# Kernel tuning notes

Measured on AMD Instinct MI355X. Metric: run time of the kernel, lower is better.

Reference implementation:

```python
import jax, jax.numpy as jnp
import numpy as np

B, S, D, H, FF = 2, 2048, 1024, 16, 4096
DH = D // H  # per-head dim = 64
EPS = 1e-5


def layer_norm(x, g, b):
    mu = jnp.mean(x, axis=-1, keepdims=True)
    var = jnp.mean((x - mu) ** 2, axis=-1, keepdims=True)
    return (x - mu) * jax.lax.rsqrt(var + EPS) * g + b


def setup_inputs() -> dict:
    key = jax.random.key(0)
    ks = jax.random.split(key, 12)
    s_in = 1.0 / np.sqrt(D)
    s_ff = 1.0 / np.sqrt(FF)
    return {
        "x": jax.random.normal(ks[0], (B, S, D), jnp.float32),
        # per-head projections stacked over heads: [H, D, DH]
        "Wq": jax.random.normal(ks[1], (H, D, DH), jnp.float32) * s_in,
        "bq": jnp.zeros((H, DH), jnp.float32),
        "Wk": jax.random.normal(ks[2], (H, D, DH), jnp.float32) * s_in,
        "bk": jnp.zeros((H, DH), jnp.float32),
        "Wv": jax.random.normal(ks[3], (H, D, DH), jnp.float32) * s_in,
        "bv": jnp.zeros((H, DH), jnp.float32),
        "ln1_g": jnp.ones((D,), jnp.float32),
        "ln1_b": jnp.zeros((D,), jnp.float32),
        "ln2_g": jnp.ones((D,), jnp.float32),
        "ln2_b": jnp.zeros((D,), jnp.float32),
        "W1": jax.random.normal(ks[4], (D, FF), jnp.float32) * s_in,
        "b1": jnp.zeros((FF,), jnp.float32),
        "W2": jax.random.normal(ks[5], (FF, D), jnp.float32) * s_ff,
        "b2": jnp.zeros((D,), jnp.float32),
    }


def reference(x, Wq, bq, Wk, bk, Wv, bv, ln1_g, ln1_b, ln2_g, ln2_b, W1, b1, W2, b2):
    # --- attention sub-block (pre-LN) ---
    h = layer_norm(x, ln1_g, ln1_b)                      # [B,S,D]
    q = jnp.einsum('bsd,hde->bhse', h, Wq) + bq[None, :, None, :]
    k = jnp.einsum('bsd,hde->bhse', h, Wk) + bk[None, :, None, :]
    v = jnp.einsum('bsd,hde->bhse', h, Wv) + bv[None, :, None, :]
    score = jnp.einsum('bhse,bhte->bhst', q, k) / jnp.sqrt(jnp.float32(DH))
    causal = jnp.tril(jnp.ones((S, S), bool))            # lower-triangular mask
    score = jnp.where(causal, score, -jnp.inf)
    attn = jax.nn.softmax(score, axis=-1)                # [B,H,S,S]
    o = jnp.einsum('bhst,bhte->bhse', attn, v)           # [B,H,S,DH]
    o = jnp.transpose(o, (0, 2, 1, 3)).reshape(B, S, D)  # concat heads
    x = x + o
    # --- FFN sub-block (pre-LN) ---
    h2 = layer_norm(x, ln2_g, ln2_b)
    f = jax.nn.gelu(h2 @ W1 + b1, approximate=False) @ W2 + b2
    return x + f
```

## Files before the change

kernel.cpp:

```cpp
#include <hip/hip_runtime.h>
#include <hip/hip_bf16.h>
#include <cstdint>
#include <cstddef>


typedef short bf16x8 __attribute__((ext_vector_type(8)));
typedef float f32x4 __attribute__((ext_vector_type(4)));

#define DEV static __device__ __forceinline__

DEV unsigned short f2bf(float f) {
  union { float fv; unsigned u; } a; a.fv = f;
  unsigned r = a.u + 0x7FFFu + ((a.u >> 16) & 1u);
  return (unsigned short)(r >> 16);
}

DEV void gload_lds16(const void* g, void* l) {
  __builtin_amdgcn_global_load_lds(
      (const __attribute__((address_space(1))) unsigned int*)g,
      (__attribute__((address_space(3))) unsigned int*)l,
      16, 0, 0);
}

__global__ __launch_bounds__(256) void k_transpose(const float* __restrict__ in,
                                                   unsigned short* __restrict__ out,
                                                   int R, int C,
                                                   long inBatchStride, long outBatchStride) {
  __shared__ float tile[32][33];
  long batch = blockIdx.z;
  int c0 = blockIdx.x * 32;
  int r0 = blockIdx.y * 32;
  const float* src = in + batch * inBatchStride;
  unsigned short* dst = out + batch * outBatchStride;
  int tx = threadIdx.x, ty = threadIdx.y;
  #pragma unroll
  for (int i = ty; i < 32; i += 8)
    tile[i][tx] = src[(long)(r0 + i) * C + (c0 + tx)];
  __syncthreads();
  #pragma unroll
  for (int i = ty; i < 32; i += 8)
    dst[(long)(c0 + i) * R + (r0 + tx)] = f2bf(tile[tx][i]);
}

__global__ void k_concat_bias(const float* __restrict__ bq, const float* __restrict__ bk,
                              const float* __restrict__ bv, float* __restrict__ out) {
  int i = blockIdx.x * 256 + threadIdx.x;
  if (i < 1024) out[i] = bq[i];
  else if (i < 2048) out[i] = bk[i - 1024];
  else if (i < 3072) out[i] = bv[i - 2048];
}

__global__ __launch_bounds__(256) void k_ln_bf16(const float* __restrict__ x,
                                                 const float* __restrict__ g,
                                                 const float* __restrict__ b,
                                                 unsigned short* __restrict__ out) {
  int row = blockIdx.x;
  const float* xr = x + (size_t)row * 1024;
  int t = threadIdx.x;
  float4 v = *(const float4*)(xr + t * 4);
  float s = v.x + v.y + v.z + v.w;
  float s2 = v.x * v.x + v.y * v.y + v.z * v.z + v.w * v.w;
  for (int off = 32; off > 0; off >>= 1) {
    s  += __shfl_down(s,  off, 64);
    s2 += __shfl_down(s2, off, 64);
  }
  __shared__ float ws1[4], ws2[4];
  __shared__ float mu_s, rs_s;
  int wid = t >> 6, lane = t & 63;
  if (lane == 0) { ws1[wid] = s; ws2[wid] = s2; }
  __syncthreads();
  if (t == 0) {
    float S1 = ws1[0] + ws1[1] + ws1[2] + ws1[3];
    float S2 = ws2[0] + ws2[1] + ws2[2] + ws2[3];
    float mu = S1 * (1.0f / 1024.0f);
    float var = S2 * (1.0f / 1024.0f) - mu * mu;
    mu_s = mu;
    rs_s = rsqrtf(var + 1e-5f);
  }
  __syncthreads();
  float mu = mu_s, rs = rs_s;
  float4 gv = *(const float4*)(g + t * 4);
  float4 bv = *(const float4*)(b + t * 4);
  ushort4 o;
  o.x = f2bf((v.x - mu) * rs * gv.x + bv.x);
  o.y = f2bf((v.y - mu) * rs * gv.y + bv.y);
  o.z = f2bf((v.z - mu) * rs * gv.z + bv.z);
  o.w = f2bf((v.w - mu) * rs * gv.w + bv.w);
  *(ushort4*)(out + (size_t)row * 1024 + t * 4) = o;
}

template <int EPI>
__global__ __launch_bounds__(256) void k_gemm_bt(const unsigned short* __restrict__ A,
                                                 const unsigned short* __restrict__ Bt,
                                                 const float* __restrict__ bias,
                                                 void* __restrict__ Cout,
                                                 int M, int N, int K,
                                                 int nbx, int nby, int kparts) {
  __shared__ __align__(16) unsigned short As[128 * 64];
  __shared__ __align__(16) unsigned short Bs[128 * 64];
  int tid = threadIdx.x;

  int nwg = nbx * nby * kparts;
  int flat = blockIdx.x;
  int swz = (flat & 7) * (nwg >> 3) + (flat >> 3);
  int bx = swz % nbx;
  int rest = swz / nbx;
  int by = rest % nby;
  int kp = rest / nby;
  int col0 = bx * 128;
  int row0 = by * 128;
  int kLen = K / kparts;
  int kBeg = kp * kLen;

  int wid = tid >> 6, lane = tid & 63;
  int wr = wid >> 1, wc = wid & 1;
  int lrow = lane & 15;
  int g = lane >> 4;
  int s_row = tid >> 3;
  int s_scol = ((tid & 7) ^ (s_row & 7)) * 8;

  f32x4 acc[4][4];
  f32x4 zero = {0.f, 0.f, 0.f, 0.f};
  #pragma unroll
  for (int m = 0; m < 4; ++m)
    #pragma unroll
    for (int n = 0; n < 4; ++n) acc[m][n] = zero;

  for (int k0 = kBeg; k0 < kBeg + kLen; k0 += 64) {
    #pragma unroll
    for (int i = 0; i < 4; ++i) {
      int r = i * 32 + s_row;
      gload_lds16(A  + (size_t)(row0 + r) * K + k0 + s_scol, (char*)As + i * 4096 + tid * 16);
      gload_lds16(Bt + (size_t)(col0 + r) * K + k0 + s_scol, (char*)Bs + i * 4096 + tid * 16);
    }
    __syncthreads();
    bf16x8 af[4][2], bf[4][2];
    #pragma unroll
    for (int m = 0; m < 4; ++m) {
      int ra = wr * 64 + m * 16 + lrow;
      #pragma unroll
      for (int kk = 0; kk < 2; ++kk) {
        int byteoff = ra * 128 + (((kk * 4 + g) ^ (lrow & 7)) << 4);
        af[m][kk] = *(const bf16x8*)((const char*)As + byteoff);
      }
    }
    #pragma unroll
    for (int n = 0; n < 4; ++n) {
      int rb = wc * 64 + n * 16 + lrow;
      #pragma unroll
      for (int kk = 0; kk < 2; ++kk) {
        int byteoff = rb * 128 + (((kk * 4 + g) ^ (lrow & 7)) << 4);
        bf[n][kk] = *(const bf16x8*)((const char*)Bs + byteoff);
      }
    }
    #pragma unroll
    for (int m = 0; m < 4; ++m)
      #pragma unroll
      for (int n = 0; n < 4; ++n)
        #pragma unroll
        for (int kk = 0; kk < 2; ++kk)
          acc[m][n] = __builtin_amdgcn_mfma_f32_16x16x32_bf16(af[m][kk], bf[n][kk], acc[m][n], 0, 0, 0);
    __syncthreads();
  }

  int rbase = row0 + wr * 64 + g * 4;
  int cbase = col0 + wc * 64 + lrow;
  #pragma unroll
  for (int m = 0; m < 4; ++m) {
    #pragma unroll
    for (int n = 0; n < 4; ++n) {
      int col = cbase + n * 16;
      float bia = bias[col];
      #pragma unroll
      for (int j = 0; j < 4; ++j) {
        int row = rbase + m * 16 + j;
        float v = acc[m][n][j];
        if constexpr (EPI == 0) {
          ((unsigned short*)Cout)[(size_t)row * N + col] = f2bf(v + bia);
        } else if constexpr (EPI == 1) {
          float u = v + bia;
          float gel = 0.5f * u * (1.0f + erff(u * 0.70710678118f));
          ((unsigned short*)Cout)[(size_t)row * N + col] = f2bf(gel);
        } else {
          float u = v + (kp == 0 ? bia : 0.0f);
          atomicAdd((float*)Cout + (size_t)row * N + col, u);
        }
      }
    }
  }
}

__global__ __launch_bounds__(256) void k_flash_attn(const unsigned short* __restrict__ qkv,
                                                    const float* __restrict__ x,
                                                    float* __restrict__ out) {
  int blk = blockIdx.x;
  int pairIdx = blk & 15;
  int bh = blk >> 4;
  int b = bh >> 4, h = bh & 15;
  const int LDQ = 3072;
  int tb = b * 2048;
  int qcol = h * 64, kcol = 1024 + h * 64, vcol = 2048 + h * 64;
  int tid = threadIdx.x, wid = tid >> 6, lane = tid & 63;
  int lrow = lane & 15;
  int g = lane >> 4;
  int kgrp = g * 8;

  __shared__ __align__(16) unsigned short Ks[2][64 * 64];
  __shared__ __align__(16) unsigned short Vt[2][64 * 64];
  __shared__ __align__(16) unsigned short Pl[4][16 * 64];

  int s_row = tid >> 3;
  int s_srccol = ((tid & 7) ^ ((tid >> 3) & 7)) * 8;

  unsigned short* myP = &Pl[wid][0];
  f32x4 zero = {0.f, 0.f, 0.f, 0.f};

  for (int half = 0; half < 2; ++half) {
    int qt = (half == 0) ? pairIdx : 31 - pairIdx;
    int q0 = qt * 64;
    int nkv = qt + 1;

    bf16x8 aq[2];
    #pragma unroll
    for (int kk = 0; kk < 2; ++kk)
      aq[kk] = *(const bf16x8*)(qkv + (size_t)(tb + q0 + wid * 16 + lrow) * LDQ + qcol + kk * 32 + kgrp);

    f32x4 oacc[4];
    #pragma unroll
    for (int e = 0; e < 4; ++e) oacc[e] = zero;
    float mrun[4], lrun[4];
    #pragma unroll
    for (int r = 0; r < 4; ++r) { mrun[r] = -1e30f; lrun[r] = 0.0f; }

    int cur = 0;
    bf16x8 vreg[2];

    #pragma unroll
    for (int i = 0; i < 2; ++i)
      gload_lds16(qkv + (size_t)(tb + i * 32 + s_row) * LDQ + kcol + s_srccol,
                  (char*)Ks[0] + i * 4096 + tid * 16);
    #pragma unroll
    for (int i = 0; i < 2; ++i) {
      int chunk = i * 256 + tid;
      vreg[i] = *(const bf16x8*)(qkv + (size_t)(tb + (chunk >> 3)) * LDQ + vcol + (chunk & 7) * 8);
    }
    #pragma unroll
    for (int i = 0; i < 2; ++i) {
      int chunk = i * 256 + tid;
      int t = chunk >> 3, e0 = (chunk & 7) * 8;
      #pragma unroll
      for (int jj = 0; jj < 8; ++jj) {
        int e = e0 + jj;
        int byteoff = e * 128 + ((((t >> 3) ^ (e & 7) ^ (e >> 3)) & 7) << 4) + (t & 7) * 2;
        *(unsigned short*)((char*)Vt[0] + byteoff) = (unsigned short)vreg[i][jj];
      }
    }

    for (int j = 0; j < nkv; ++j) {
      __syncthreads();
      int nxt = cur ^ 1;
      bool pf = (j + 1 < nkv);
      if (pf) {
        #pragma unroll
        for (int i = 0; i < 2; ++i)
          gload_lds16(qkv + (size_t)(tb + (j + 1) * 64 + i * 32 + s_row) * LDQ + kcol + s_srccol,
                      (char*)Ks[nxt] + i * 4096 + tid * 16);
        #pragma unroll
        for (int i = 0; i < 2; ++i) {
          int chunk = i * 256 + tid;
          vreg[i] = *(const bf16x8*)(qkv + (size_t)(tb + (j + 1) * 64 + (chunk >> 3)) * LDQ + vcol + (chunk & 7) * 8);
        }
      }

      f32x4 sacc[4];
      #pragma unroll
      for (int n = 0; n < 4; ++n) sacc[n] = zero;
      __builtin_amdgcn_s_setprio(1);
      #pragma unroll
      for (int n = 0; n < 4; ++n) {
        int trow = n * 16 + lrow;
        #pragma unroll
        for (int kk = 0; kk < 2; ++kk) {
          int byteoff = trow * 128 + (((kk * 4 + g) ^ (trow & 7)) << 4);
          bf16x8 bk = *(const bf16x8*)((const char*)Ks[cur] + byteoff);
          sacc[n] = __builtin_amdgcn_mfma_f32_16x16x32_bf16(aq[kk], bk, sacc[n], 0, 0, 0);
        }
      }
      __builtin_amdgcn_s_setprio(0);

      bool diag = (j == qt);
      float pv[4][4];
      #pragma unroll
      for (int r = 0; r < 4; ++r) {
        int sg = q0 + wid * 16 + g * 4 + r;
        float mx = -1e30f;
        #pragma unroll
        for (int n = 0; n < 4; ++n) {
          float sv = sacc[n][r] * 0.125f;
          int tg = j * 64 + n * 16 + lrow;
          if (diag && tg > sg) sv = -1e30f;
          pv[r][n] = sv;
          mx = fmaxf(mx, sv);
        }
        #pragma unroll
        for (int off = 1; off < 16; off <<= 1) mx = fmaxf(mx, __shfl_xor(mx, off, 64));
        float mnew = fmaxf(mrun[r], mx);
        float esc = __expf(mrun[r] - mnew);
        float rsum = 0.f;
        #pragma unroll
        for (int n = 0; n < 4; ++n) {
          float p = __expf(pv[r][n] - mnew);
          pv[r][n] = p;
          rsum += p;
        }
        #pragma unroll
        for (int off = 1; off < 16; off <<= 1) rsum += __shfl_xor(rsum, off, 64);
        lrun[r] = lrun[r] * esc + rsum;
        mrun[r] = mnew;
        #pragma unroll
        for (int e = 0; e < 4; ++e) oacc[e][r] *= esc;
      }

      if (pf) {
        #pragma unroll
        for (int i = 0; i < 2; ++i) {
          int chunk = i * 256 + tid;
          int t = chunk >> 3, e0 = (chunk & 7) * 8;
          #pragma unroll
          for (int jj = 0; jj < 8; ++jj) {
            int e = e0 + jj;
            int byteoff = e * 128 + ((((t >> 3) ^ (e & 7) ^ (e >> 3)) & 7) << 4) + (t & 7) * 2;
            *(unsigned short*)((char*)Vt[nxt] + byteoff) = (unsigned short)vreg[i][jj];
          }
        }
      }

      #pragma unroll
      for (int r = 0; r < 4; ++r) {
        int q = g * 4 + r;
        #pragma unroll
        for (int n = 0; n < 4; ++n) {
          int t = n * 16 + lrow;
          int byteoff = q * 128 + ((((t >> 3) ^ (q & 7)) & 7) << 4) + (t & 7) * 2;
          *(unsigned short*)((char*)myP + byteoff) = f2bf(pv[r][n]);
        }
      }

      __builtin_amdgcn_s_setprio(1);
      #pragma unroll
      for (int kk = 0; kk < 2; ++kk) {
        int pbyte = lrow * 128 + (((kk * 4 + g) ^ (lrow & 7)) << 4);
        bf16x8 ap = *(const bf16x8*)((const char*)myP + pbyte);
        #pragma unroll
        for (int e = 0; e < 4; ++e) {
          int erow = e * 16 + lrow;
          int vbyte = erow * 128 + ((((kk * 4 + g) ^ (erow & 7) ^ (erow >> 3)) & 7) << 4);
          bf16x8 bv = *(const bf16x8*)((const char*)Vt[cur] + vbyte);
          oacc[e] = __builtin_amdgcn_mfma_f32_16x16x32_bf16(ap, bv, oacc[e], 0, 0, 0);
        }
      }
      __builtin_amdgcn_s_setprio(0);
      cur = nxt;
    }

    #pragma unroll
    for (int r = 0; r < 4; ++r) {
      float inv = 1.0f / lrun[r];
      int row = tb + q0 + wid * 16 + g * 4 + r;
      #pragma unroll
      for (int e = 0; e < 4; ++e) {
        size_t idx = (size_t)row * 1024 + h * 64 + e * 16 + lrow;
        out[idx] = x[idx] + oacc[e][r] * inv;
      }
    }
  }
}

extern "C" void kernel_launch(void* const* d_in, const int* in_sizes, int n_in,
                              void* d_out, int out_size, void* d_ws, size_t ws_size,
                              hipStream_t stream) {
  (void)in_sizes; (void)n_in; (void)out_size; (void)ws_size;
  const float* x    = (const float*)d_in[0];
  const float* Wq   = (const float*)d_in[1];
  const float* bq   = (const float*)d_in[2];
  const float* Wk   = (const float*)d_in[3];
  const float* bk   = (const float*)d_in[4];
  const float* Wv   = (const float*)d_in[5];
  const float* bv   = (const float*)d_in[6];
  const float* ln1g = (const float*)d_in[7];
  const float* ln1b = (const float*)d_in[8];
  const float* ln2g = (const float*)d_in[9];
  const float* ln2b = (const float*)d_in[10];
  const float* W1   = (const float*)d_in[11];
  const float* b1   = (const float*)d_in[12];
  const float* W2   = (const float*)d_in[13];
  const float* b2   = (const float*)d_in[14];
  float* out = (float*)d_out;
  char* ws = (char*)d_ws;

  unsigned short* h1    = (unsigned short*)(ws + 0);
  unsigned short* wqkvT = (unsigned short*)(ws + 8388608);
  unsigned short* w1T   = (unsigned short*)(ws + 14680064);
  unsigned short* w2T   = (unsigned short*)(ws + 23068672);
  float*          bqkv  = (float*)(ws + 31457280);
  unsigned short* qkv   = (unsigned short*)(ws + 33554432);
  unsigned short* fbuf  = (unsigned short*)(ws + 33554432);

  dim3 tb(32, 8);
  k_transpose<<<dim3(2, 32, 16), tb, 0, stream>>>(Wq, wqkvT,               1024, 64, 1024L * 64, 64L * 1024);
  k_transpose<<<dim3(2, 32, 16), tb, 0, stream>>>(Wk, wqkvT + 1024 * 1024, 1024, 64, 1024L * 64, 64L * 1024);
  k_transpose<<<dim3(2, 32, 16), tb, 0, stream>>>(Wv, wqkvT + 2048 * 1024, 1024, 64, 1024L * 64, 64L * 1024);
  k_transpose<<<dim3(128, 32, 1), tb, 0, stream>>>(W1, w1T, 1024, 4096, 0, 0);
  k_transpose<<<dim3(32, 128, 1), tb, 0, stream>>>(W2, w2T, 4096, 1024, 0, 0);
  k_concat_bias<<<12, 256, 0, stream>>>(bq, bk, bv, bqkv);

  k_ln_bf16<<<4096, 256, 0, stream>>>(x, ln1g, ln1b, h1);
  k_gemm_bt<0><<<768, 256, 0, stream>>>(h1, wqkvT, bqkv, qkv, 4096, 3072, 1024, 24, 32, 1);
  k_flash_attn<<<512, 256, 0, stream>>>(qkv, x, out);
  k_ln_bf16<<<4096, 256, 0, stream>>>(out, ln2g, ln2b, h1);
  k_gemm_bt<1><<<1024, 256, 0, stream>>>(h1, w1T, b1, fbuf, 4096, 4096, 1024, 32, 32, 1);
  k_gemm_bt<2><<<512, 256, 0, stream>>>(fbuf, w2T, b2, out, 4096, 1024, 4096, 8, 32, 2);
}
```

Measured before the change: 392.1 us.

## Write V transposed from QKV GEMM epilogue and async-load it in attention

```diff
diff --git a/kernel.cpp b/kernel.cpp
--- a/kernel.cpp
+++ b/kernel.cpp
@@ -94,6 +94,7 @@
                                                  const unsigned short* __restrict__ Bt,
                                                  const float* __restrict__ bias,
                                                  void* __restrict__ Cout,
+                                                 void* __restrict__ Cout2,
                                                  int M, int N, int K,
                                                  int nbx, int nby, int kparts) {
   __shared__ __align__(16) unsigned short As[128 * 64];
@@ -181,9 +182,20 @@
           float u = v + bia;
           float gel = 0.5f * u * (1.0f + erff(u * 0.70710678118f));
           ((unsigned short*)Cout)[(size_t)row * N + col] = f2bf(gel);
-        } else {
+        } else if constexpr (EPI == 2) {
           float u = v + (kp == 0 ? bia : 0.0f);
           atomicAdd((float*)Cout + (size_t)row * N + col, u);
+        } else {
+          unsigned short bfv = f2bf(v + bia);
+          if (col < 2048) {
+            ((unsigned short*)Cout)[(size_t)row * 2048 + col] = bfv;
+          } else {
+            int e = col & 63;
+            int head = (col >> 6) & 15;
+            int bb = row >> 11;
+            int t = row & 2047;
+            ((unsigned short*)Cout2)[(((size_t)bb * 16 + head) * 64 + e) * 2048 + t] = bfv;
+          }
         }
       }
     }
@@ -191,26 +203,28 @@
 }
 
 __global__ __launch_bounds__(256) void k_flash_attn(const unsigned short* __restrict__ qkv,
+                                                    const unsigned short* __restrict__ vT,
                                                     const float* __restrict__ x,
                                                     float* __restrict__ out) {
   int blk = blockIdx.x;
   int pairIdx = blk & 15;
   int bh = blk >> 4;
   int b = bh >> 4, h = bh & 15;
-  const int LDQ = 3072;
+  const int LDQ = 2048;
   int tb = b * 2048;
-  int qcol = h * 64, kcol = 1024 + h * 64, vcol = 2048 + h * 64;
+  int qcol = h * 64, kcol = 1024 + h * 64;
+  const unsigned short* vbase = vT + (size_t)bh * 64 * 2048;
   int tid = threadIdx.x, wid = tid >> 6, lane = tid & 63;
   int lrow = lane & 15;
   int g = lane >> 4;
   int kgrp = g * 8;
 
   __shared__ __align__(16) unsigned short Ks[2][64 * 64];
-  __shared__ __align__(16) unsigned short Vt[2][64 * 64];
+  __shared__ __align__(16) unsigned short Vs[2][64 * 64];
   __shared__ __align__(16) unsigned short Pl[4][16 * 64];
 
   int s_row = tid >> 3;
-  int s_srccol = ((tid & 7) ^ ((tid >> 3) & 7)) * 8;
+  int s_scol = ((tid & 7) ^ ((tid >> 3) & 7)) * 8;
 
   unsigned short* myP = &Pl[wid][0];
   f32x4 zero = {0.f, 0.f, 0.f, 0.f};
@@ -233,42 +247,26 @@
     for (int r = 0; r < 4; ++r) { mrun[r] = -1e30f; lrun[r] = 0.0f; }
 
     int cur = 0;
-    bf16x8 vreg[2];
-
-    #pragma unroll
-    for (int i = 0; i < 2; ++i)
-      gload_lds16(qkv + (size_t)(tb + i * 32 + s_row) * LDQ + kcol + s_srccol,
+
+    __syncthreads();
+    #pragma unroll
+    for (int i = 0; i < 2; ++i) {
+      gload_lds16(qkv + (size_t)(tb + i * 32 + s_row) * LDQ + kcol + s_scol,
                   (char*)Ks[0] + i * 4096 + tid * 16);
-    #pragma unroll
-    for (int i = 0; i < 2; ++i) {
-      int chunk = i * 256 + tid;
-      vreg[i] = *(const bf16x8*)(qkv + (size_t)(tb + (chunk >> 3)) * LDQ + vcol + (chunk & 7) * 8);
-    }
-    #pragma unroll
-    for (int i = 0; i < 2; ++i) {
-      int chunk = i * 256 + tid;
-      int t = chunk >> 3, e0 = (chunk & 7) * 8;
-      #pragma unroll
-      for (int jj = 0; jj < 8; ++jj) {
-        int e = e0 + jj;
-        int byteoff = e * 128 + ((((t >> 3) ^ (e & 7) ^ (e >> 3)) & 7) << 4) + (t & 7) * 2;
-        *(unsigned short*)((char*)Vt[0] + byteoff) = (unsigned short)vreg[i][jj];
-      }
+      gload_lds16(vbase + (size_t)(i * 32 + s_row) * 2048 + s_scol,
+                  (char*)Vs[0] + i * 4096 + tid * 16);
     }
 
     for (int j = 0; j < nkv; ++j) {
       __syncthreads();
       int nxt = cur ^ 1;
-      bool pf = (j + 1 < nkv);
-      if (pf) {
-        #pragma unroll
-        for (int i = 0; i < 2; ++i)
-          gload_lds16(qkv + (size_t)(tb + (j + 1) * 64 + i * 32 + s_row) * LDQ + kcol + s_srccol,
+      if (j + 1 < nkv) {
+        #pragma unroll
+        for (int i = 0; i < 2; ++i) {
+          gload_lds16(qkv + (size_t)(tb + (j + 1) * 64 + i * 32 + s_row) * LDQ + kcol + s_scol,
                       (char*)Ks[nxt] + i * 4096 + tid * 16);
-        #pragma unroll
-        for (int i = 0; i < 2; ++i) {
-          int chunk = i * 256 + tid;
-          vreg[i] = *(const bf16x8*)(qkv + (size_t)(tb + (j + 1) * 64 + (chunk >> 3)) * LDQ + vcol + (chunk & 7) * 8);
+          gload_lds16(vbase + (size_t)(i * 32 + s_row) * 2048 + (j + 1) * 64 + s_scol,
+                      (char*)Vs[nxt] + i * 4096 + tid * 16);
         }
       }
 
@@ -321,20 +319,6 @@
         for (int e = 0; e < 4; ++e) oacc[e][r] *= esc;
       }
 
-      if (pf) {
-        #pragma unroll
-        for (int i = 0; i < 2; ++i) {
-          int chunk = i * 256 + tid;
-          int t = chunk >> 3, e0 = (chunk & 7) * 8;
-          #pragma unroll
-          for (int jj = 0; jj < 8; ++jj) {
-            int e = e0 + jj;
-            int byteoff = e * 128 + ((((t >> 3) ^ (e & 7) ^ (e >> 3)) & 7) << 4) + (t & 7) * 2;
-            *(unsigned short*)((char*)Vt[nxt] + byteoff) = (unsigned short)vreg[i][jj];
-          }
-        }
-      }
-
       #pragma unroll
       for (int r = 0; r < 4; ++r) {
         int q = g * 4 + r;
@@ -354,8 +338,8 @@
         #pragma unroll
         for (int e = 0; e < 4; ++e) {
           int erow = e * 16 + lrow;
-          int vbyte = erow * 128 + ((((kk * 4 + g) ^ (erow & 7) ^ (erow >> 3)) & 7) << 4);
-          bf16x8 bv = *(const bf16x8*)((const char*)Vt[cur] + vbyte);
+          int vbyte = erow * 128 + (((kk * 4 + g) ^ (erow & 7)) << 4);
+          bf16x8 bv = *(const bf16x8*)((const char*)Vs[cur] + vbyte);
           oacc[e] = __builtin_amdgcn_mfma_f32_16x16x32_bf16(ap, bv, oacc[e], 0, 0, 0);
         }
       }
@@ -404,6 +388,7 @@
   unsigned short* w2T   = (unsigned short*)(ws + 23068672);
   float*          bqkv  = (float*)(ws + 31457280);
   unsigned short* qkv   = (unsigned short*)(ws + 33554432);
+  unsigned short* vT    = (unsigned short*)(ws + 50331648);
   unsigned short* fbuf  = (unsigned short*)(ws + 33554432);
 
   dim3 tb(32, 8);
@@ -415,9 +400,9 @@
   k_concat_bias<<<12, 256, 0, stream>>>(bq, bk, bv, bqkv);
 
   k_ln_bf16<<<4096, 256, 0, stream>>>(x, ln1g, ln1b, h1);
-  k_gemm_bt<0><<<768, 256, 0, stream>>>(h1, wqkvT, bqkv, qkv, 4096, 3072, 1024, 24, 32, 1);
-  k_flash_attn<<<512, 256, 0, stream>>>(qkv, x, out);
+  k_gemm_bt<3><<<768, 256, 0, stream>>>(h1, wqkvT, bqkv, qkv, vT, 4096, 3072, 1024, 24, 32, 1);
+  k_flash_attn<<<512, 256, 0, stream>>>(qkv, vT, x, out);
   k_ln_bf16<<<4096, 256, 0, stream>>>(out, ln2g, ln2b, h1);
-  k_gemm_bt<1><<<1024, 256, 0, stream>>>(h1, w1T, b1, fbuf, 4096, 4096, 1024, 32, 32, 1);
-  k_gemm_bt<2><<<512, 256, 0, stream>>>(fbuf, w2T, b2, out, 4096, 1024, 4096, 8, 32, 2);
-}
+  k_gemm_bt<1><<<1024, 256, 0, stream>>>(h1, w1T, b1, fbuf, nullptr, 4096, 4096, 1024, 32, 32, 1);
+  k_gemm_bt<2><<<512, 256, 0, stream>>>(fbuf, w2T, b2, out, nullptr, 4096, 1024, 4096, 8, 32, 2);
+}
```

Result: no change. 388.2 us (-1.0%).
